# Kernel tuning notes

Measured on AMD Instinct MI355X. Metric: run time of the kernel, lower is better.

## Reference

```python
import jax, jax.numpy as jnp
import numpy as np

BETA = 0.9
THRESH = 1.0
SLOPE = 25.0  # snntorch fast_sigmoid default slope
T = 4096

@jax.custom_vjp
def spike_fn(x):
    # Heaviside forward, fast-sigmoid surrogate backward
    return (x > 0).astype(x.dtype)

def _spike_fwd(x):
    return (x > 0).astype(x.dtype), x

def _spike_bwd(x, g):
    return (g / (SLOPE * jnp.abs(x) + 1.0) ** 2,)

spike_fn.defvjp(_spike_fwd, _spike_bwd)

def setup_inputs():
    key = jax.random.key(0)
    ks = jax.random.split(key, 5)
    B = 1024
    x = jax.random.normal(ks[0], (B, 6, T), dtype=jnp.float32)
    W1 = jax.random.normal(ks[1], (10, 6), dtype=jnp.float32) / np.sqrt(6.0)
    b1 = jax.random.normal(ks[2], (10,), dtype=jnp.float32) * 0.01
    W2 = jax.random.normal(ks[3], (27, 10), dtype=jnp.float32) / np.sqrt(10.0)
    b2 = jax.random.normal(ks[4], (27,), dtype=jnp.float32) * 0.01
    return {"x": x, "W1": W1, "b1": b1, "W2": W2, "b2": b2}

def reference(x, W1, b1, W2, b2):
    B = x.shape[0]
    xt = jnp.transpose(x, (2, 0, 1))  # [T, B, 6]
    mem1_0 = jnp.zeros((B, 10), x.dtype)
    mem2_0 = jnp.zeros((B, 27), x.dtype)

    def step(carry, xin):
        mem1, mem2 = carry
        cur1 = xin @ W1.T + b1                              # [B,10]
        rst1 = jax.lax.stop_gradient((mem1 > THRESH).astype(x.dtype))
        mem1 = BETA * mem1 + cur1 - rst1 * THRESH           # subtract reset
        spk1 = spike_fn(mem1 - THRESH)
        cur2 = spk1 @ W2.T + b2                             # [B,27]
        rst2 = jax.lax.stop_gradient((mem2 > THRESH).astype(x.dtype))
        mem2 = BETA * mem2 + cur2 - rst2 * THRESH
        return (mem1, mem2), None

    (mem1, mem2), _ = jax.lax.scan(step, (mem1_0, mem2_0), xt)
    # module returns only the spike of the final timestep
    return spike_fn(mem2 - THRESH)
```

## Files before the change

kernel.cpp:

```cpp
#include <hip/hip_runtime.h>


#define T_STEPS 4096
#define BETA 0.9f
#define THRESH 1.0f
#define CH 64
#define NCHUNK (T_STEPS / CH)
#define GRP 8
#define NGRP (CH / GRP)

__global__ __launch_bounds__(64, 1) void snn_kernel(
    const float* __restrict__ x,
    const float* __restrict__ W1,
    const float* __restrict__ b1,
    const float* __restrict__ W2,
    const float* __restrict__ b2,
    float* __restrict__ out)
{
    __shared__ float tabLo[32 * 32];
    __shared__ float tabHi[32 * 32];
    __shared__ float curBuf[10 * 68];

    const int l = threadIdx.x;
    const int b = blockIdx.x;

    if (l < 32) {
        for (int j = 0; j < 27; ++j) {
            float slo = b2[j];
            float shi = 0.0f;
            #pragma unroll
            for (int i = 0; i < 5; ++i) {
                if (l & (1 << i)) {
                    slo += W2[j * 10 + i];
                    shi += W2[j * 10 + 5 + i];
                }
            }
            tabLo[l * 32 + j] = slo;
            tabHi[l * 32 + j] = shi;
        }
    }

    float w1r[60], b1r[10];
    #pragma unroll
    for (int i = 0; i < 10; ++i) {
        b1r[i] = b1[i];
        #pragma unroll
        for (int c = 0; c < 6; ++c) w1r[i * 6 + c] = W1[i * 6 + c];
    }

    const int ri = (l < 10) ? l : 9;
    const int rj = (l < 27) ? l : 26;

    float mem1 = 0.0f, mem2 = 0.0f;
    bool sp1 = false;
    bool sp2 = false;

    const float* xb = x + (size_t)b * 6 * T_STEPS;
    float xv[6], xn[6];
    #pragma unroll
    for (int c = 0; c < 6; ++c) xv[c] = xb[c * T_STEPS + l];

    const float* cp = &curBuf[ri * 68];

    #pragma unroll 1
    for (int k = 0; k < NCHUNK; ++k) {
        #pragma unroll
        for (int i = 0; i < 10; ++i) {
            float acc = xv[0] * w1r[i * 6 + 0];
            acc = fmaf(xv[1], w1r[i * 6 + 1], acc);
            acc = fmaf(xv[2], w1r[i * 6 + 2], acc);
            acc = fmaf(xv[3], w1r[i * 6 + 3], acc);
            acc = fmaf(xv[4], w1r[i * 6 + 4], acc);
            acc = fmaf(xv[5], w1r[i * 6 + 5], acc);
            curBuf[i * 68 + l] = acc + b1r[i];
        }

        if (k + 1 < NCHUNK) {
            #pragma unroll
            for (int c = 0; c < 6; ++c) xn[c] = xb[c * T_STEPS + (k + 1) * CH + l];
        }

        unsigned mlo[GRP], mhi[GRP];

        {
            float4 q0 = *(const float4*)(cp + 0);
            float4 q1 = *(const float4*)(cp + 4);
            float c1v[8] = {q0.x, q0.y, q0.z, q0.w, q1.x, q1.y, q1.z, q1.w};
            #pragma unroll
            for (int s = 0; s < 8; ++s) {
                float t1 = fmaf(BETA, mem1, c1v[s]);
                mem1 = sp1 ? (t1 - THRESH) : t1;
                sp1 = mem1 > THRESH;
                unsigned m = (unsigned)__ballot(sp1);
                mlo[s] = (m & 31u) << 5;
                mhi[s] = ((m >> 5) & 31u) << 5;
            }
        }

        #pragma unroll
        for (int g = 0; g < NGRP; ++g) {
            const bool more = (g + 1 < NGRP);

            float c1n[8];
            if (more) {
                float4 p0 = *(const float4*)(cp + (g + 1) * 8);
                float4 p1 = *(const float4*)(cp + (g + 1) * 8 + 4);
                c1n[0] = p0.x; c1n[1] = p0.y; c1n[2] = p0.z; c1n[3] = p0.w;
                c1n[4] = p1.x; c1n[5] = p1.y; c1n[6] = p1.z; c1n[7] = p1.w;
            }

            float tlo[8], thi[8];
            #pragma unroll
            for (int s = 0; s < 8; ++s) {
                tlo[s] = tabLo[mlo[s] + rj];
                thi[s] = tabHi[mhi[s] + rj];
            }

            unsigned nlo[GRP], nhi[GRP];
            if (more) {
                #pragma unroll
                for (int s = 0; s < 8; ++s) {
                    float t1 = fmaf(BETA, mem1, c1n[s]);
                    mem1 = sp1 ? (t1 - THRESH) : t1;
                    sp1 = mem1 > THRESH;
                    unsigned m = (unsigned)__ballot(sp1);
                    nlo[s] = (m & 31u) << 5;
                    nhi[s] = ((m >> 5) & 31u) << 5;
                }
            }

            #pragma unroll
            for (int s = 0; s < 8; ++s) {
                float cur2 = tlo[s] + thi[s];
                float t2 = fmaf(BETA, mem2, cur2);
                mem2 = sp2 ? (t2 - THRESH) : t2;
                sp2 = mem2 > THRESH;
            }

            if (more) {
                #pragma unroll
                for (int s = 0; s < 8; ++s) { mlo[s] = nlo[s]; mhi[s] = nhi[s]; }
            }
        }

        if (k + 1 < NCHUNK) {
            #pragma unroll
            for (int c = 0; c < 6; ++c) xv[c] = xn[c];
        }
    }

    if (l < 27) {
        out[b * 27 + l] = sp2 ? 1.0f : 0.0f;
    }
}

extern "C" void kernel_launch(void* const* d_in, const int* in_sizes, int n_in,
                              void* d_out, int out_size, void* d_ws, size_t ws_size,
                              hipStream_t stream) {
    const float* x  = (const float*)d_in[0];
    const float* W1 = (const float*)d_in[1];
    const float* b1 = (const float*)d_in[2];
    const float* W2 = (const float*)d_in[3];
    const float* b2 = (const float*)d_in[4];
    float* out = (float*)d_out;

    const int B = in_sizes[0] / (6 * T_STEPS);
    snn_kernel<<<dim3(B), dim3(64), 0, stream>>>(x, W1, b1, W2, b2, out);
}
```

Before: 310.1 us.

## Split layer-1 and layer-2 recurrences into producer/consumer wavefronts

The block now has two wavefronts. Wave 0 computes layer-1 currents and membrane recurrence and writes the per-step spike masks to a double-buffered shared array. Wave 1 consumes the previous chunk's masks through readlane, with table lookups prefetched, to run the layer-2 recurrence. Running the two serial dependency chains concurrently is meant to shorten the critical path per timestep. In exchange it adds a block barrier per chunk and doubles the threads per block.

```diff
diff --git a/kernel.cpp b/kernel.cpp
--- a/kernel.cpp
+++ b/kernel.cpp
@@ -9,7 +9,7 @@
 #define GRP 8
 #define NGRP (CH / GRP)
 
-__global__ __launch_bounds__(64, 1) void snn_kernel(
+__global__ __launch_bounds__(128, 1) void snn_kernel(
     const float* __restrict__ x,
     const float* __restrict__ W1,
     const float* __restrict__ b1,
@@ -20,136 +20,163 @@
     __shared__ float tabLo[32 * 32];
     __shared__ float tabHi[32 * 32];
     __shared__ float curBuf[10 * 68];
+    __shared__ unsigned maskBuf[2][64];
 
-    const int l = threadIdx.x;
-    const int b = blockIdx.x;
+    const int tid = threadIdx.x;
+    const int wid = tid >> 6;
+    const int l   = tid & 63;
+    const int b   = blockIdx.x;
 
-    if (l < 32) {
+    if (tid < 32) {
         for (int j = 0; j < 27; ++j) {
             float slo = b2[j];
             float shi = 0.0f;
             #pragma unroll
             for (int i = 0; i < 5; ++i) {
-                if (l & (1 << i)) {
+                if (tid & (1 << i)) {
                     slo += W2[j * 10 + i];
                     shi += W2[j * 10 + 5 + i];
                 }
             }
-            tabLo[l * 32 + j] = slo;
-            tabHi[l * 32 + j] = shi;
+            tabLo[tid * 32 + j] = slo;
+            tabHi[tid * 32 + j] = shi;
         }
     }
 
     float w1r[60], b1r[10];
-    #pragma unroll
-    for (int i = 0; i < 10; ++i) {
-        b1r[i] = b1[i];
+    float xv[6], xn[6];
+    float mem1 = 0.0f;
+    bool  sp1 = false;
+    const int ri = (l < 10) ? l : 9;
+    const float* cp = &curBuf[ri * 68];
+    const float* xb = x + (size_t)b * 6 * T_STEPS;
+
+    if (wid == 0) {
         #pragma unroll
-        for (int c = 0; c < 6; ++c) w1r[i * 6 + c] = W1[i * 6 + c];
+        for (int i = 0; i < 10; ++i) {
+            b1r[i] = b1[i];
+            #pragma unroll
+            for (int c = 0; c < 6; ++c) w1r[i * 6 + c] = W1[i * 6 + c];
+        }
+        #pragma unroll
+        for (int c = 0; c < 6; ++c) xv[c] = xb[c * T_STEPS + l];
     }
 
-    const int ri = (l < 10) ? l : 9;
+    float mem2 = 0.0f;
+    bool  sp2 = false;
     const int rj = (l < 27) ? l : 26;
 
-    float mem1 = 0.0f, mem2 = 0.0f;
-    bool sp1 = false;
-    bool sp2 = false;
-
-    const float* xb = x + (size_t)b * 6 * T_STEPS;
-    float xv[6], xn[6];
-    #pragma unroll
-    for (int c = 0; c < 6; ++c) xv[c] = xb[c * T_STEPS + l];
-
-    const float* cp = &curBuf[ri * 68];
+    __syncthreads();
 
     #pragma unroll 1
-    for (int k = 0; k < NCHUNK; ++k) {
-        #pragma unroll
-        for (int i = 0; i < 10; ++i) {
-            float acc = xv[0] * w1r[i * 6 + 0];
-            acc = fmaf(xv[1], w1r[i * 6 + 1], acc);
-            acc = fmaf(xv[2], w1r[i * 6 + 2], acc);
-            acc = fmaf(xv[3], w1r[i * 6 + 3], acc);
-            acc = fmaf(xv[4], w1r[i * 6 + 4], acc);
-            acc = fmaf(xv[5], w1r[i * 6 + 5], acc);
-            curBuf[i * 68 + l] = acc + b1r[i];
+    for (int k = 0; k <= NCHUNK; ++k) {
+        if (wid == 0 && k < NCHUNK) {
+            #pragma unroll
+            for (int i = 0; i < 10; ++i) {
+                float acc = xv[0] * w1r[i * 6 + 0];
+                acc = fmaf(xv[1], w1r[i * 6 + 1], acc);
+                acc = fmaf(xv[2], w1r[i * 6 + 2], acc);
+                acc = fmaf(xv[3], w1r[i * 6 + 3], acc);
+                acc = fmaf(xv[4], w1r[i * 6 + 4], acc);
+                acc = fmaf(xv[5], w1r[i * 6 + 5], acc);
+                curBuf[i * 68 + l] = acc + b1r[i];
+            }
+            if (k + 1 < NCHUNK) {
+                #pragma unroll
+                for (int c = 0; c < 6; ++c) xn[c] = xb[c * T_STEPS + (k + 1) * CH + l];
+            }
+
+            unsigned vmask = 0u;
+            float c1v[8];
+            {
+                float4 q0 = *(const float4*)(cp + 0);
+                float4 q1 = *(const float4*)(cp + 4);
+                c1v[0] = q0.x; c1v[1] = q0.y; c1v[2] = q0.z; c1v[3] = q0.w;
+                c1v[4] = q1.x; c1v[5] = q1.y; c1v[6] = q1.z; c1v[7] = q1.w;
+            }
+            #pragma unroll
+            for (int g = 0; g < NGRP; ++g) {
+                float c1n[8];
+                if (g + 1 < NGRP) {
+                    float4 p0 = *(const float4*)(cp + (g + 1) * 8);
+                    float4 p1 = *(const float4*)(cp + (g + 1) * 8 + 4);
+                    c1n[0] = p0.x; c1n[1] = p0.y; c1n[2] = p0.z; c1n[3] = p0.w;
+                    c1n[4] = p1.x; c1n[5] = p1.y; c1n[6] = p1.z; c1n[7] = p1.w;
+                }
+                #pragma unroll
+                for (int s = 0; s < 8; ++s) {
+                    float t1 = fmaf(BETA, mem1, c1v[s]);
+                    mem1 = sp1 ? (t1 - THRESH) : t1;
+                    sp1 = mem1 > THRESH;
+                    unsigned m = (unsigned)__ballot(sp1);
+                    vmask = (l == g * 8 + s) ? m : vmask;
+                }
+                if (g + 1 < NGRP) {
+                    #pragma unroll
+                    for (int s = 0; s < 8; ++s) c1v[s] = c1n[s];
+                }
+            }
+            maskBuf[k & 1][l] = vmask;
         }
 
-        if (k + 1 < NCHUNK) {
-            #pragma unroll
-            for (int c = 0; c < 6; ++c) xn[c] = xb[c * T_STEPS + (k + 1) * CH + l];
-        }
+        if (wid == 1 && k >= 1) {
+            unsigned vmask = maskBuf[(k - 1) & 1][l];
 
-        unsigned mlo[GRP], mhi[GRP];
-
-        {
-            float4 q0 = *(const float4*)(cp + 0);
-            float4 q1 = *(const float4*)(cp + 4);
-            float c1v[8] = {q0.x, q0.y, q0.z, q0.w, q1.x, q1.y, q1.z, q1.w};
+            unsigned mlo[GRP], mhi[GRP];
+            float tlo[GRP], thi[GRP];
             #pragma unroll
             for (int s = 0; s < 8; ++s) {
-                float t1 = fmaf(BETA, mem1, c1v[s]);
-                mem1 = sp1 ? (t1 - THRESH) : t1;
-                sp1 = mem1 > THRESH;
-                unsigned m = (unsigned)__ballot(sp1);
+                unsigned m = (unsigned)__builtin_amdgcn_readlane((int)vmask, s);
                 mlo[s] = (m & 31u) << 5;
                 mhi[s] = ((m >> 5) & 31u) << 5;
             }
-        }
-
-        #pragma unroll
-        for (int g = 0; g < NGRP; ++g) {
-            const bool more = (g + 1 < NGRP);
-
-            float c1n[8];
-            if (more) {
-                float4 p0 = *(const float4*)(cp + (g + 1) * 8);
-                float4 p1 = *(const float4*)(cp + (g + 1) * 8 + 4);
-                c1n[0] = p0.x; c1n[1] = p0.y; c1n[2] = p0.z; c1n[3] = p0.w;
-                c1n[4] = p1.x; c1n[5] = p1.y; c1n[6] = p1.z; c1n[7] = p1.w;
-            }
-
-            float tlo[8], thi[8];
             #pragma unroll
             for (int s = 0; s < 8; ++s) {
                 tlo[s] = tabLo[mlo[s] + rj];
                 thi[s] = tabHi[mhi[s] + rj];
             }
 
-            unsigned nlo[GRP], nhi[GRP];
-            if (more) {
+            #pragma unroll
+            for (int g = 0; g < NGRP; ++g) {
+                unsigned nlo[GRP], nhi[GRP];
+                float ntl[GRP], nth[GRP];
+                if (g + 1 < NGRP) {
+                    #pragma unroll
+                    for (int s = 0; s < 8; ++s) {
+                        unsigned m = (unsigned)__builtin_amdgcn_readlane(
+                            (int)vmask, (g + 1) * 8 + s);
+                        nlo[s] = (m & 31u) << 5;
+                        nhi[s] = ((m >> 5) & 31u) << 5;
+                    }
+                    #pragma unroll
+                    for (int s = 0; s < 8; ++s) {
+                        ntl[s] = tabLo[nlo[s] + rj];
+                        nth[s] = tabHi[nhi[s] + rj];
+                    }
+                }
                 #pragma unroll
                 for (int s = 0; s < 8; ++s) {
-                    float t1 = fmaf(BETA, mem1, c1n[s]);
-                    mem1 = sp1 ? (t1 - THRESH) : t1;
-                    sp1 = mem1 > THRESH;
-                    unsigned m = (unsigned)__ballot(sp1);
-                    nlo[s] = (m & 31u) << 5;
-                    nhi[s] = ((m >> 5) & 31u) << 5;
+                    float cur2 = tlo[s] + thi[s];
+                    float t2 = fmaf(BETA, mem2, cur2);
+                    mem2 = sp2 ? (t2 - THRESH) : t2;
+                    sp2 = mem2 > THRESH;
                 }
-            }
-
-            #pragma unroll
-            for (int s = 0; s < 8; ++s) {
-                float cur2 = tlo[s] + thi[s];
-                float t2 = fmaf(BETA, mem2, cur2);
-                mem2 = sp2 ? (t2 - THRESH) : t2;
-                sp2 = mem2 > THRESH;
-            }
-
-            if (more) {
-                #pragma unroll
-                for (int s = 0; s < 8; ++s) { mlo[s] = nlo[s]; mhi[s] = nhi[s]; }
+                if (g + 1 < NGRP) {
+                    #pragma unroll
+                    for (int s = 0; s < 8; ++s) { tlo[s] = ntl[s]; thi[s] = nth[s]; }
+                }
             }
         }
 
-        if (k + 1 < NCHUNK) {
+        if (wid == 0 && k + 1 < NCHUNK) {
             #pragma unroll
             for (int c = 0; c < 6; ++c) xv[c] = xn[c];
         }
+
+        __syncthreads();
     }
 
-    if (l < 27) {
+    if (wid == 1 && l < 27) {
         out[b * 27 + l] = sp2 ? 1.0f : 0.0f;
     }
 }
@@ -165,5 +192,5 @@
     float* out = (float*)d_out;
 
     const int B = in_sizes[0] / (6 * T_STEPS);
-    snn_kernel<<<dim3(B), dim3(64), 0, stream>>>(x, W1, b1, W2, b2, out);
+    snn_kernel<<<dim3(B), dim3(128), 0, stream>>>(x, W1, b1, W2, b2, out);
 }
```

After: 312.7 us. About the same (+0.9%).
